# Performance work log

Measured on AMD Instinct MI355X. Metric: run time of the kernel, lower is better.

## Reference

```python
import jax, jax.numpy as jnp
import numpy as np

KERNEL_NUM = 20

def _l2norm(x):
    # torch F.normalize: x / max(||x||, eps)
    n = jnp.sqrt(jnp.sum(x * x, axis=-1, keepdims=True))
    return x / jnp.maximum(n, 1e-12)

def setup_inputs() -> dict:
    key = jax.random.key(0)
    ks = jax.random.split(key, 5)
    B, C, H, S, E, V = 32, 5, 50, 20, 300, 60000
    return {
        "candidate_title": jax.random.randint(ks[0], (B, C, S), 0, V),
        "clicked_title": jax.random.randint(ks[1], (B, H, S), 0, V),
        "candidate_title_pad": jnp.ones((B, C, S), jnp.float32),
        "clicked_title_pad": jnp.ones((B, H, S), jnp.float32),
        "embedding": jax.random.normal(ks[2], (V, E), jnp.float32),
        "ltr_w": jax.random.normal(ks[3], (H * KERNEL_NUM, 1), jnp.float32) * 0.03,
        "ltr_b": jax.random.normal(ks[4], (1,), jnp.float32),
    }

def reference(candidate_title, clicked_title, candidate_title_pad, clicked_title_pad, embedding, ltr_w, ltr_b):
    B, C, S = candidate_title.shape
    H = clicked_title.shape[1]
    K = KERNEL_NUM
    dt = embedding.dtype
    mus = (-0.9 + 0.1 * jnp.arange(K, dtype=dt))                    # [K]
    sigmas = jnp.concatenate([jnp.full((K - 1,), 0.1, dt), jnp.full((1,), 0.001, dt)])
    cdd = _l2norm(embedding[candidate_title])                        # [B,C,S,E]
    his = _l2norm(embedding[clicked_title])                          # [B,H,S,E]
    sim = jnp.einsum('bcse,bhte->bchst', cdd, his)                   # [B,C,H,S,S]
    mask_his = clicked_title_pad[:, None, :, None, :, None]          # [B,1,H,1,S,1]
    mask_cdd = candidate_title_pad[:, :, None, :, None]              # [B,C,1,S,1]
    kern = jnp.exp(-((sim[..., None] - mus) ** 2) / (2.0 * sigmas ** 2)) * mask_his  # [B,C,H,S,S,K]
    pooling_sum = jnp.sum(kern, axis=4)                              # [B,C,H,S,K]
    log_pooling = jnp.log(jnp.clip(pooling_sum, 1e-10, None)) * mask_cdd * 0.01
    pooling_vectors = jnp.sum(log_pooling, axis=-2)                  # [B,C,H,K]
    score = pooling_vectors.reshape(B, C, H * K) @ ltr_w + ltr_b     # [B,C,1]
    score = jax.nn.log_softmax(score, axis=1)                        # cdd_size > 1 path
    return jnp.squeeze(score)                                        # [B,C]
```

## Files before the change

kernel.cpp:

```cpp
#include <hip/hip_runtime.h>
#include <hip/hip_fp16.h>

typedef _Float16 half8 __attribute__((ext_vector_type(8)));
typedef _Float16 half4v __attribute__((ext_vector_type(4)));
typedef float float4v __attribute__((ext_vector_type(4)));

#define E_DIM 300
#define KP 320
#define B_ 32
#define NROW_CDD 3200
#define NROW_HIS 32000

__global__ __launch_bounds__(256) void gather_norm(const int* __restrict__ cand,
                                                   const int* __restrict__ clk,
                                                   const float* __restrict__ emb,
                                                   _Float16* __restrict__ outH)
{
    int row  = blockIdx.x * 4 + (threadIdx.x >> 6);
    int lane = threadIdx.x & 63;
    int tok = (row < NROW_CDD) ? cand[row] : clk[row - NROW_CDD];
    const float4* e4 = (const float4*)(emb + (size_t)tok * E_DIM);

    float4 v0 = e4[lane];
    float4 v1 = {0.f, 0.f, 0.f, 0.f};
    if (lane < 11) v1 = e4[64 + lane];
    float ss = v0.x*v0.x + v0.y*v0.y + v0.z*v0.z + v0.w*v0.w
             + v1.x*v1.x + v1.y*v1.y + v1.z*v1.z + v1.w*v1.w;
#pragma unroll
    for (int off = 32; off; off >>= 1) ss += __shfl_xor(ss, off);
    float sc = 1.0f / fmaxf(sqrtf(ss), 1e-12f);

    _Float16* o = outH + (size_t)row * KP;
    half4v h0 = { (_Float16)(v0.x*sc), (_Float16)(v0.y*sc), (_Float16)(v0.z*sc), (_Float16)(v0.w*sc) };
    *(half4v*)(o + 4 * lane) = h0;
    if (lane < 11) {
        half4v h1 = { (_Float16)(v1.x*sc), (_Float16)(v1.y*sc), (_Float16)(v1.z*sc), (_Float16)(v1.w*sc) };
        *(half4v*)(o + 256 + 4 * lane) = h1;
    } else if (lane < 16) {
        half4v hz = { (_Float16)0.f, (_Float16)0.f, (_Float16)0.f, (_Float16)0.f };
        *(half4v*)(o + 256 + 4 * lane) = hz;
    }
}

__global__ __launch_bounds__(448, 2) void sim_gemm(const _Float16* __restrict__ wsH,
                                                   _Float16* __restrict__ simW)
{
    __shared__ __align__(16) char Bbuf[64 * 640 + 128];
    __shared__ _Float16 simT[100 * 66];

    int b = blockIdx.y, ntile = blockIdx.x;
    int tid = threadIdx.x;
    int wave = tid >> 6, lane = tid & 63;
    int g4 = lane >> 4, r16 = lane & 15;

    const char* gA = (const char*)(wsH + (size_t)b * 100 * KP);
    const char* gB = (const char*)(wsH + (size_t)(NROW_CDD + b * 1000) * KP);

    int rA = wave * 16 + r16; if (rA > 99) rA = 99;
    const char* pA = gA + (size_t)rA * 640;
    half8 af[10];
#pragma unroll
    for (int k = 0; k < 10; ++k) af[k] = *(const half8*)(pA + k * 64 + g4 * 16);

    uint4 bv[6];
#pragma unroll
    for (int j = 0; j < 6; ++j) {
        int u = tid + 448 * j; if (u > 2559) u = 2559;
        int r = u / 40;
        int gr = ntile * 64 + r; if (gr > 999) gr = 999;
        bv[j] = *(const uint4*)(gB + (size_t)(gr * 40 + (u - r * 40)) * 16);
    }
#pragma unroll
    for (int j = 0; j < 6; ++j) {
        int u = tid + 448 * j;
        if (u < 2560) {
            int r = u / 40;
            *(uint4*)(Bbuf + ((u * 16) ^ ((r & 7) << 4))) = bv[j];
        }
    }
    __syncthreads();

    float4v acc[4];
#pragma unroll
    for (int n = 0; n < 4; ++n) acc[n] = (float4v){0.f, 0.f, 0.f, 0.f};

#pragma unroll
    for (int k = 0; k < 10; ++k) {
#pragma unroll
        for (int n = 0; n < 4; ++n) {
            int rB = n * 16 + r16;
            half8 bf = *(const half8*)(Bbuf + ((rB * 640 + k * 64 + g4 * 16) ^ ((rB & 7) << 4)));
            acc[n] = __builtin_amdgcn_mfma_f32_16x16x32_f16(af[k], bf, acc[n], 0, 0, 0);
        }
    }

#pragma unroll
    for (int n = 0; n < 4; ++n) {
#pragma unroll
        for (int j = 0; j < 4; ++j) {
            int r = wave * 16 + g4 * 4 + j;
            if (r < 100) simT[r * 66 + n * 16 + r16] = (_Float16)acc[n][j];
        }
    }
    __syncthreads();

    for (int u = tid; u < 6400; u += 448) {
        int r = u >> 6, c = u & 63;
        int gcol = ntile * 64 + c;
        if (gcol < 1000) simW[(size_t)(b * 100 + r) * 1000 + gcol] = simT[r * 66 + c];
    }
}

__global__ __launch_bounds__(256) void knrm_pool(const _Float16* __restrict__ simW,
                                                 const float* __restrict__ cpad,
                                                 const float* __restrict__ hpad,
                                                 const float* __restrict__ ltr_w,
                                                 float* __restrict__ rowsum)
{
    __shared__ float sS[50 * 21];
    __shared__ float mS[50 * 21];
    __shared__ float wS[1000];
    __shared__ float part[4];

    int row = blockIdx.x;
    int b = row / 100;
    int tid = threadIdx.x;

    if (tid < 250) {
        int p = tid * 4;
        half4v hv = *(const half4v*)(simW + (size_t)row * 1000 + p);
        float4v mv = *(const float4v*)(hpad + (size_t)b * 1000 + p);
        *(float4v*)&wS[p] = *(const float4v*)(ltr_w + p);
#pragma unroll
        for (int q = 0; q < 4; ++q) {
            int pq = p + q, h = pq / 20, t = pq - h * 20;
            sS[h * 21 + t] = (float)hv[q];
            mS[h * 21 + t] = mv[q];
        }
    }
    __syncthreads();

    float val = 0.f;
    if (tid < 250) {
        int h = tid % 50, kq = tid / 50;
        float bj[4], cj[4];
        bool is19[4];
#pragma unroll
        for (int j = 0; j < 4; ++j) {
            float mu = -0.9f + 0.1f * (float)(kq * 4 + j);
            bj[j] = 100.0f * mu;
            cj[j] = -50.0f * mu * mu;
            is19[j] = (kq * 4 + j) == 19;
        }
        float psum0 = 0.f, psum1 = 0.f, psum2 = 0.f, psum3 = 0.f;
        const float* sp = sS + h * 21;
        const float* mp = mS + h * 21;
#pragma unroll 4
        for (int t = 0; t < 20; ++t) {
            float s  = sp[t];
            float mm = mp[t];
            float d  = s - 1.0f;
            float arg19 = -500000.0f * d * d;
            float a0 = is19[0] ? arg19 : fmaf(fmaf(-50.0f, s, bj[0]), s, cj[0]);
            float a1 = is19[1] ? arg19 : fmaf(fmaf(-50.0f, s, bj[1]), s, cj[1]);
            float a2 = is19[2] ? arg19 : fmaf(fmaf(-50.0f, s, bj[2]), s, cj[2]);
            float a3 = is19[3] ? arg19 : fmaf(fmaf(-50.0f, s, bj[3]), s, cj[3]);
            psum0 = fmaf(__expf(a0), mm, psum0);
            psum1 = fmaf(__expf(a1), mm, psum1);
            psum2 = fmaf(__expf(a2), mm, psum2);
            psum3 = fmaf(__expf(a3), mm, psum3);
        }
        const float* wp = wS + h * 20 + kq * 4;
        val  = __logf(fmaxf(psum0, 1e-10f)) * wp[0];
        val += __logf(fmaxf(psum1, 1e-10f)) * wp[1];
        val += __logf(fmaxf(psum2, 1e-10f)) * wp[2];
        val += __logf(fmaxf(psum3, 1e-10f)) * wp[3];
    }
#pragma unroll
    for (int off = 32; off; off >>= 1) val += __shfl_down(val, off);
    int wave = tid >> 6, lane = tid & 63;
    if (lane == 0) part[wave] = val;
    __syncthreads();
    if (tid == 0)
        rowsum[row] = (part[0] + part[1] + part[2] + part[3]) * 0.01f * cpad[row];
}

__global__ __launch_bounds__(64) void finalize(const float* __restrict__ rowsum,
                                               const float* __restrict__ ltr_b,
                                               float* __restrict__ out)
{
    int b = blockIdx.x;
    int tid = threadIdx.x;
    __shared__ float sc[5];
    if (tid < 5) {
        float a = ltr_b[0];
        const float* rp = rowsum + (b * 5 + tid) * 20;
#pragma unroll
        for (int s = 0; s < 20; ++s) a += rp[s];
        sc[tid] = a;
    }
    __syncthreads();
    if (tid < 5) {
        float m = fmaxf(fmaxf(fmaxf(sc[0], sc[1]), fmaxf(sc[2], sc[3])), sc[4]);
        float sum = 0.f;
#pragma unroll
        for (int i = 0; i < 5; ++i) sum += __expf(sc[i] - m);
        out[b * 5 + tid] = sc[tid] - m - __logf(sum);
    }
}

extern "C" void kernel_launch(void* const* d_in, const int* in_sizes, int n_in,
                              void* d_out, int out_size, void* d_ws, size_t ws_size,
                              hipStream_t stream)
{
    const int*   cand = (const int*)d_in[0];
    const int*   clk  = (const int*)d_in[1];
    const float* cpad = (const float*)d_in[2];
    const float* hpad = (const float*)d_in[3];
    const float* emb  = (const float*)d_in[4];
    const float* lw   = (const float*)d_in[5];
    const float* lb   = (const float*)d_in[6];
    float* out = (float*)d_out;

    _Float16* wsH  = (_Float16*)d_ws;
    _Float16* simW = (_Float16*)((char*)d_ws + (size_t)(NROW_CDD + NROW_HIS) * KP * 2);
    float* rowsum  = (float*)((char*)simW + (size_t)B_ * 100 * 1000 * 2);

    hipLaunchKernelGGL(gather_norm, dim3((NROW_CDD + NROW_HIS) / 4), dim3(256), 0, stream,
                       cand, clk, emb, wsH);
    hipLaunchKernelGGL(sim_gemm, dim3(16, B_), dim3(448), 0, stream, wsH, simW);
    hipLaunchKernelGGL(knrm_pool, dim3(NROW_CDD), dim3(256), 0, stream,
                       simW, cpad, hpad, lw, rowsum);
    hipLaunchKernelGGL(finalize, dim3(B_), dim3(64), 0, stream, rowsum, lb, out);
}
```

Baseline: 45.21 us.

## Fuse clicked-title gather and normalization into the similarity GEMM

The clicked-title embedding gather and L2 normalization move out of the separate gather kernel and into sim_gemm. Each GEMM block now loads fp32 embedding rows straight from the table, converts them to fp16 in shared memory, accumulates squared norms with shared-memory atomics, and scales the GEMM output by the inverse norm. This removes the write and re-read of the 32000-row normalized fp16 history buffer. In exchange there are more bytes of fp32 global loads per block, register pressure from 11 float4 loads, and atomic contention on ssAcc. Using unnormalized fp16 inputs also changes rounding slightly.

```diff
diff --git a/kernel.cpp b/kernel.cpp
--- a/kernel.cpp
+++ b/kernel.cpp
@@ -9,16 +9,14 @@
 #define KP 320
 #define B_ 32
 #define NROW_CDD 3200
-#define NROW_HIS 32000
 
 __global__ __launch_bounds__(256) void gather_norm(const int* __restrict__ cand,
-                                                   const int* __restrict__ clk,
                                                    const float* __restrict__ emb,
                                                    _Float16* __restrict__ outH)
 {
     int row  = blockIdx.x * 4 + (threadIdx.x >> 6);
     int lane = threadIdx.x & 63;
-    int tok = (row < NROW_CDD) ? cand[row] : clk[row - NROW_CDD];
+    int tok = cand[row];
     const float4* e4 = (const float4*)(emb + (size_t)tok * E_DIM);
 
     float4 v0 = e4[lane];
@@ -42,41 +40,56 @@
     }
 }
 
-__global__ __launch_bounds__(448, 2) void sim_gemm(const _Float16* __restrict__ wsH,
+__global__ __launch_bounds__(448, 2) void sim_gemm(const _Float16* __restrict__ wsA,
+                                                   const int* __restrict__ clk,
+                                                   const float* __restrict__ emb,
                                                    _Float16* __restrict__ simW)
 {
     __shared__ __align__(16) char Bbuf[64 * 640 + 128];
     __shared__ _Float16 simT[100 * 66];
+    __shared__ int tokS[64];
+    __shared__ float ssAcc[64];
 
     int b = blockIdx.y, ntile = blockIdx.x;
     int tid = threadIdx.x;
     int wave = tid >> 6, lane = tid & 63;
     int g4 = lane >> 4, r16 = lane & 15;
 
-    const char* gA = (const char*)(wsH + (size_t)b * 100 * KP);
-    const char* gB = (const char*)(wsH + (size_t)(NROW_CDD + b * 1000) * KP);
-
     int rA = wave * 16 + r16; if (rA > 99) rA = 99;
-    const char* pA = gA + (size_t)rA * 640;
+    const char* pA = (const char*)(wsA + (size_t)(b * 100 + rA) * KP);
     half8 af[10];
 #pragma unroll
     for (int k = 0; k < 10; ++k) af[k] = *(const half8*)(pA + k * 64 + g4 * 16);
 
-    uint4 bv[6];
-#pragma unroll
-    for (int j = 0; j < 6; ++j) {
-        int u = tid + 448 * j; if (u > 2559) u = 2559;
-        int r = u / 40;
-        int gr = ntile * 64 + r; if (gr > 999) gr = 999;
-        bv[j] = *(const uint4*)(gB + (size_t)(gr * 40 + (u - r * 40)) * 16);
-    }
-#pragma unroll
-    for (int j = 0; j < 6; ++j) {
+    if (tid < 64) {
+        int col = ntile * 64 + tid; if (col > 999) col = 999;
+        tokS[tid] = clk[b * 1000 + col];
+        ssAcc[tid] = 0.f;
+    }
+    __syncthreads();
+
+    float4 bv[11];
+#pragma unroll
+    for (int j = 0; j < 11; ++j) {
+        int u = tid + 448 * j; if (u > 4799) u = 4799;
+        int r = u / 75, c = u - r * 75;
+        bv[j] = *(const float4*)(emb + (size_t)tokS[r] * E_DIM + c * 4);
+    }
+#pragma unroll
+    for (int j = 0; j < 11; ++j) {
         int u = tid + 448 * j;
-        if (u < 2560) {
-            int r = u / 40;
-            *(uint4*)(Bbuf + ((u * 16) ^ ((r & 7) << 4))) = bv[j];
-        }
+        if (u < 4800) {
+            int r = u / 75, c = u - r * 75;
+            float4 v = bv[j];
+            atomicAdd(&ssAcc[r], v.x*v.x + v.y*v.y + v.z*v.z + v.w*v.w);
+            half4v h = { (_Float16)v.x, (_Float16)v.y, (_Float16)v.z, (_Float16)v.w };
+            *(half4v*)(Bbuf + ((r * 640 + c * 8) ^ ((r & 7) << 4))) = h;
+        }
+    }
+    if (tid < 320) {
+        int r = tid / 5, j5 = tid - r * 5;
+        half4v z = { (_Float16)0.f, (_Float16)0.f, (_Float16)0.f, (_Float16)0.f };
+        *(half4v*)(Bbuf + ((r * 640 + 600 + j5 * 8) ^ ((r & 7) << 4))) = z;
     }
     __syncthreads();
 
@@ -96,10 +109,11 @@
 
 #pragma unroll
     for (int n = 0; n < 4; ++n) {
+        float inv = 1.0f / fmaxf(sqrtf(ssAcc[n * 16 + r16]), 1e-12f);
 #pragma unroll
         for (int j = 0; j < 4; ++j) {
             int r = wave * 16 + g4 * 4 + j;
-            if (r < 100) simT[r * 66 + n * 16 + r16] = (_Float16)acc[n][j];
+            if (r < 100) simT[r * 66 + n * 16 + r16] = (_Float16)(acc[n][j] * inv);
         }
     }
     __syncthreads();
@@ -222,13 +236,14 @@
     const float* lb   = (const float*)d_in[6];
     float* out = (float*)d_out;
 
-    _Float16* wsH  = (_Float16*)d_ws;
-    _Float16* simW = (_Float16*)((char*)d_ws + (size_t)(NROW_CDD + NROW_HIS) * KP * 2);
+    _Float16* wsA  = (_Float16*)d_ws;
+    _Float16* simW = (_Float16*)((char*)d_ws + (size_t)NROW_CDD * KP * 2);
     float* rowsum  = (float*)((char*)simW + (size_t)B_ * 100 * 1000 * 2);
 
-    hipLaunchKernelGGL(gather_norm, dim3((NROW_CDD + NROW_HIS) / 4), dim3(256), 0, stream,
-                       cand, clk, emb, wsH);
-    hipLaunchKernelGGL(sim_gemm, dim3(16, B_), dim3(448), 0, stream, wsH, simW);
+    hipLaunchKernelGGL(gather_norm, dim3(NROW_CDD / 4), dim3(256), 0, stream,
+                       cand, emb, wsA);
+    hipLaunchKernelGGL(sim_gemm, dim3(16, B_), dim3(448), 0, stream,
+                       wsA, clk, emb, simW);
     hipLaunchKernelGGL(knrm_pool, dim3(NROW_CDD), dim3(256), 0, stream,
                        simW, cpad, hpad, lw, rowsum);
     hipLaunchKernelGGL(finalize, dim3(B_), dim3(64), 0, stream, rowsum, lb, out);
```

New measurement: 59.37 us. 31.3% more time.
